# Optimization experiments

Measured on AMD Instinct MI355X. Metric: run time of the kernel, lower is better.

The kernel has to match this reference:

```python
import jax, jax.numpy as jnp
import numpy as np

WORLD_SIZE = 4
NUM_TOKENS = 1024
TOPK = 2
NUM_EXPERTS = 8
INTER_PER_RANK = 1024  # intermediate_size (4096) // world_size (4)
HIDDEN = 2048


def setup_inputs() -> dict:
    key = jax.random.key(0)
    k1, k2, k3 = jax.random.split(key, 3)
    # per-rank shard of expert intermediate activations, expanded (token, topk) order
    intermediate_states = jax.random.normal(
        k1, (WORLD_SIZE, NUM_TOKENS * TOPK, INTER_PER_RANK), dtype=jnp.float16)
    # per-rank shard of expert down-proj weights [rank, expert, inter_per_rank, hidden]
    w = (jax.random.normal(
        k2, (WORLD_SIZE, NUM_EXPERTS, INTER_PER_RANK, HIDDEN), dtype=jnp.float32) * 0.05
        ).astype(jnp.float16)
    router_logits = jax.random.normal(k3, (NUM_TOKENS, NUM_EXPERTS), dtype=jnp.float32)
    return {"intermediate_states": intermediate_states, "w": w,
            "router_logits": router_logits, "topk": TOPK}


def reference(intermediate_states, w, router_logits, topk):
    # intermediate_states: [R, T*topk, I_pr], w: [R, E, I_pr, H], router_logits: [T, E]
    R, TK, I = intermediate_states.shape
    _, E, _, H = w.shape
    T = TK // topk

    # top-k routing: softmax over the selected top-k logits (Mixtral-style gates)
    vals, idx = jax.lax.top_k(router_logits, topk)            # [T, topk]
    gate = jax.nn.softmax(vals, axis=-1)                      # [T, topk] fp32
    # combine weights per expanded token per expert: [T*topk, E]
    comb = (jax.nn.one_hot(idx, E, dtype=jnp.float32) * gate[..., None]).reshape(TK, E)

    # grouped GEMM (dense all-expert form) with fp32 accumulation; the einsum
    # simultaneously sums the per-rank partials (the "reduce" of reduce-scatter)
    x32 = intermediate_states.astype(jnp.float32)
    w32 = w.astype(jnp.float32)
    h_all = jnp.einsum('rti,reih->teh', x32, w32)             # [T*topk, E, H]
    y = jnp.einsum('teh,te->th', h_all, comb)                 # [T*topk, H]
    y = y.reshape(T, topk, H).sum(axis=1)                     # combine top-k -> [T, H]

    # "scatter" half of reduce-scatter: each rank keeps T//R contiguous tokens
    out = y.reshape(R, T // R, H).astype(intermediate_states.dtype)
    return out
```

## Files before the change

### kernel.cpp

```cpp
#include <hip/hip_runtime.h>
#include <hip/hip_bf16.h>

#define NTOK 1024
#define TKN  2048
#define NE   8
#define NRANK 4
#define IPR  1024
#define HD   2048
#define KD   4096
#define BM   256
#define BN   64
#define BK   64
#define KSPLIT 2
#define KPS  (KD / KSPLIT)
#define NIT  (KPS / BK)
#define XS   72
#define MAXTILES 16
#define NBL  (HD / BN)
#define NWG  (MAXTILES * NBL * KSPLIT)

typedef __bf16 bf16x8 __attribute__((ext_vector_type(8)));
typedef float f32x4 __attribute__((ext_vector_type(4)));
typedef unsigned short u16x8 __attribute__((ext_vector_type(8)));

static __device__ inline unsigned short f2b(float f) {
  return __builtin_bit_cast(unsigned short, __float2bfloat16(f));
}

__global__ __launch_bounds__(256) void zero_kernel(float* __restrict__ p) {
  size_t i = ((size_t)blockIdx.x * 256 + threadIdx.x) * 4;
  *reinterpret_cast<float4*>(p + i) = float4{0.f, 0.f, 0.f, 0.f};
}

__global__ void routing_kernel(const float* __restrict__ logits,
                               float* __restrict__ gate,
                               int* __restrict__ perm,
                               int* __restrict__ tile_e,
                               int* __restrict__ tile_r0,
                               int* __restrict__ tile_nr) {
  __shared__ int cnt[NE];
  __shared__ int cur[NE];
  const int tid = threadIdx.x;
  if (tid < NE) cnt[tid] = 0;
  __syncthreads();

  float l[NE];
#pragma unroll
  for (int e = 0; e < NE; ++e) l[e] = logits[tid * NE + e];

  float v0 = l[0]; int i0 = 0;
  float v1 = -3.4e38f; int i1 = 0;
#pragma unroll
  for (int e = 1; e < NE; ++e) {
    if (l[e] > v0) { v1 = v0; i1 = i0; v0 = l[e]; i0 = e; }
    else if (l[e] > v1) { v1 = l[e]; i1 = e; }
  }
  float e1  = expf(v1 - v0);
  float inv = 1.0f / (1.0f + e1);
  gate[2 * tid]     = inv;
  gate[2 * tid + 1] = e1 * inv;

  atomicAdd(&cnt[i0], 1);
  atomicAdd(&cnt[i1], 1);
  __syncthreads();

  if (tid == 0) {
    int run = 0, nt = 0;
    for (int e = 0; e < NE; ++e) {
      cur[e] = run;
      int c = cnt[e];
      for (int r0 = 0; r0 < c; r0 += BM) {
        tile_e[nt]  = e;
        tile_r0[nt] = run + r0;
        tile_nr[nt] = (c - r0 < BM) ? (c - r0) : BM;
        ++nt;
      }
      run += c;
    }
    for (; nt < MAXTILES; ++nt) tile_e[nt] = -1;
  }
  __syncthreads();

  int p0 = atomicAdd(&cur[i0], 1); perm[p0] = 2 * tid;
  int p1 = atomicAdd(&cur[i1], 1); perm[p1] = 2 * tid + 1;
}

__global__ __launch_bounds__(512, 4) void gemm_kernel(
    const float* __restrict__ x,
    const float* __restrict__ w,
    const int* __restrict__ perm,
    const int* __restrict__ tile_e,
    const int* __restrict__ tile_r0,
    const int* __restrict__ tile_nr,
    const float* __restrict__ gate,
    float* __restrict__ out) {
  const int id = blockIdx.x;
  const int sw = (id & 7) * (NWG / 8) + (id >> 3);
  const int tile = sw % MAXTILES;
  const int rem  = sw / MAXTILES;
  const int nb   = rem % NBL;
  const int ksp  = rem / NBL;

  const int e = tile_e[tile];
  if (e < 0) return;
  const int row0 = tile_r0[tile];
  const int nr   = tile_nr[tile];
  const int n0   = nb * BN;
  const int kbase = ksp * KPS;

  __shared__ unsigned short Xs[BM][XS];
  __shared__ unsigned short Ws[BN][XS];

  const int tid  = threadIdx.x;
  const int lane = tid & 63;
  const int wid  = tid >> 6;
  const int wr   = wid >> 1;
  const int wc   = wid & 1;

  const int xr = tid >> 3;
  const int xc = (tid & 7) << 3;
  int xtk[4];
#pragma unroll
  for (int p = 0; p < 4; ++p) {
    const int row = p * 64 + xr;
    xtk[p] = (row < nr) ? perm[row0 + row] : -1;
  }

  const int wn  = tid & 63;
  const int wkq = (tid >> 6) << 3;

  float4 xf[4][2];
  float  wv[8];

#define LOADREGS(KT) do {                                                        \
    const int r_  = (KT) >> 10;                                                  \
    const int i0_ = (KT) & 1023;                                                 \
    _Pragma("unroll")                                                            \
    for (int p_ = 0; p_ < 4; ++p_) {                                             \
      if (xtk[p_] >= 0) {                                                        \
        const float* sp_ = x + ((size_t)r_ * TKN + xtk[p_]) * IPR + i0_ + xc;    \
        xf[p_][0] = *reinterpret_cast<const float4*>(sp_);                       \
        xf[p_][1] = *reinterpret_cast<const float4*>(sp_ + 4);                   \
      } else {                                                                   \
        xf[p_][0] = float4{0.f, 0.f, 0.f, 0.f};                                  \
        xf[p_][1] = float4{0.f, 0.f, 0.f, 0.f};                                  \
      }                                                                          \
    }                                                                            \
    const float* wp_ = w + (((size_t)r_ * NE + e) * IPR + i0_ + wkq) * HD + n0 + wn; \
    _Pragma("unroll")                                                            \
    for (int j_ = 0; j_ < 8; ++j_) wv[j_] = wp_[(size_t)j_ * HD];                \
  } while (0)

  f32x4 acc[4][2];
#pragma unroll
  for (int a = 0; a < 4; ++a)
#pragma unroll
    for (int b = 0; b < 2; ++b) acc[a][b] = f32x4{0.f, 0.f, 0.f, 0.f};

  const int lrow = lane & 15;
  const int lk   = (lane >> 4) << 3;

  LOADREGS(kbase);

  for (int t = 0; t < NIT; ++t) {
    __syncthreads();

#pragma unroll
    for (int p = 0; p < 4; ++p) {
      u16x8 v;
      v[0] = f2b(xf[p][0].x); v[1] = f2b(xf[p][0].y);
      v[2] = f2b(xf[p][0].z); v[3] = f2b(xf[p][0].w);
      v[4] = f2b(xf[p][1].x); v[5] = f2b(xf[p][1].y);
      v[6] = f2b(xf[p][1].z); v[7] = f2b(xf[p][1].w);
      *reinterpret_cast<u16x8*>(&Xs[p * 64 + xr][xc]) = v;
    }
    {
      u16x8 a;
      a[0] = f2b(wv[0]); a[1] = f2b(wv[1]); a[2] = f2b(wv[2]); a[3] = f2b(wv[3]);
      a[4] = f2b(wv[4]); a[5] = f2b(wv[5]); a[6] = f2b(wv[6]); a[7] = f2b(wv[7]);
      *reinterpret_cast<u16x8*>(&Ws[wn][wkq]) = a;
    }
    __syncthreads();

    if (t + 1 < NIT) LOADREGS(kbase + (t + 1) * BK);

#pragma unroll
    for (int ks = 0; ks < 2; ++ks) {
      bf16x8 af[4], bfr[2];
#pragma unroll
      for (int mi = 0; mi < 4; ++mi)
        af[mi] = __builtin_bit_cast(bf16x8,
            *reinterpret_cast<const u16x8*>(&Xs[wr * 64 + mi * 16 + lrow][ks * 32 + lk]));
#pragma unroll
      for (int ni = 0; ni < 2; ++ni)
        bfr[ni] = __builtin_bit_cast(bf16x8,
            *reinterpret_cast<const u16x8*>(&Ws[wc * 32 + ni * 16 + lrow][ks * 32 + lk]));
#pragma unroll
      for (int mi = 0; mi < 4; ++mi)
#pragma unroll
        for (int ni = 0; ni < 2; ++ni)
          acc[mi][ni] = __builtin_amdgcn_mfma_f32_16x16x32_bf16(af[mi], bfr[ni], acc[mi][ni], 0, 0, 0);
    }
  }

  const int mb = (lane >> 4) << 2;
#pragma unroll
  for (int mi = 0; mi < 4; ++mi) {
#pragma unroll
    for (int q = 0; q < 4; ++q) {
      const int m = wr * 64 + mi * 16 + mb + q;
      if (m < nr) {
        const int tk = perm[row0 + m];
        const float g = gate[tk];
        float* dst = out + (size_t)(tk >> 1) * HD + n0 + wc * 32 + (lane & 15);
#pragma unroll
        for (int ni = 0; ni < 2; ++ni)
          atomicAdd(&dst[ni * 16], g * acc[mi][ni][q]);
      }
    }
  }
#undef LOADREGS
}

extern "C" void kernel_launch(void* const* d_in, const int* in_sizes, int n_in,
                              void* d_out, int out_size, void* d_ws, size_t ws_size,
                              hipStream_t stream) {
  const float* x      = (const float*)d_in[0];
  const float* w      = (const float*)d_in[1];
  const float* logits = (const float*)d_in[2];

  char* ws = (char*)d_ws;
  float* gate    = (float*)(ws + 0);
  int*   perm    = (int*)(ws + 8192);
  int*   tile_e  = (int*)(ws + 16384);
  int*   tile_r0 = (int*)(ws + 16384 + 256);
  int*   tile_nr = (int*)(ws + 16384 + 512);

  float* outf = (float*)d_out;

  zero_kernel<<<(NTOK * HD / 4) / 256, 256, 0, stream>>>(outf);
  routing_kernel<<<1, 1024, 0, stream>>>(logits, gate, perm, tile_e, tile_r0, tile_nr);
  gemm_kernel<<<NWG, 512, 0, stream>>>(x, w, perm, tile_e, tile_r0, tile_nr, gate, outf);
}
```

Baseline: 184.5 us.

## Widen N tile, convert to bf16 at load, replace atomics with workspace combine

Doubles the N tile width to 128 so each workgroup reuses its gathered X tile across more columns, halving the number of workgroups and the redundant X reads. The fp32-to-bf16 conversion moves into the global-load step so fewer registers are held across the compute phase. When enough workspace is available, each split-K/expert partial is stored plainly into a per-split expanded buffer, and a separate combine kernel applies the gates and sums. This replaces float atomics and the zero kernel, at the cost of writing and re-reading about 32 MB of workspace and launching one more kernel.

```diff
diff --git a/kernel.cpp b/kernel.cpp
--- a/kernel.cpp
+++ b/kernel.cpp
@@ -9,7 +9,7 @@
 #define HD   2048
 #define KD   4096
 #define BM   256
-#define BN   64
+#define BN   128
 #define BK   64
 #define KSPLIT 2
 #define KPS  (KD / KSPLIT)
@@ -18,6 +18,9 @@
 #define MAXTILES 16
 #define NBL  (HD / BN)
 #define NWG  (MAXTILES * NBL * KSPLIT)
+
+#define WS_YEXP_OFF 32768
+#define WS_NEED ((size_t)WS_YEXP_OFF + (size_t)KSPLIT * TKN * HD * 4)
 
 typedef __bf16 bf16x8 __attribute__((ext_vector_type(8)));
 typedef float f32x4 __attribute__((ext_vector_type(4)));
@@ -85,6 +88,7 @@
   int p1 = atomicAdd(&cur[i1], 1); perm[p1] = 2 * tid + 1;
 }
 
+template <int WSP>
 __global__ __launch_bounds__(512, 4) void gemm_kernel(
     const float* __restrict__ x,
     const float* __restrict__ w,
@@ -93,13 +97,13 @@
     const int* __restrict__ tile_r0,
     const int* __restrict__ tile_nr,
     const float* __restrict__ gate,
+    float* __restrict__ yexp,
     float* __restrict__ out) {
   const int id = blockIdx.x;
   const int sw = (id & 7) * (NWG / 8) + (id >> 3);
-  const int tile = sw % MAXTILES;
-  const int rem  = sw / MAXTILES;
-  const int nb   = rem % NBL;
-  const int ksp  = rem / NBL;
+  const int tile = sw & (MAXTILES - 1);
+  const int nb   = (sw >> 4) & (NBL - 1);
+  const int ksp  = sw >> 8;
 
   const int e = tile_e[tile];
   if (e < 0) return;
@@ -126,11 +130,11 @@
     xtk[p] = (row < nr) ? perm[row0 + row] : -1;
   }
 
-  const int wn  = tid & 63;
-  const int wkq = (tid >> 6) << 3;
-
-  float4 xf[4][2];
-  float  wv[8];
+  const int wn  = tid & 127;
+  const int wkg = (tid >> 7) << 4;
+
+  u16x8 xpk[4];
+  u16x8 wpk[2];
 
 #define LOADREGS(KT) do {                                                        \
     const int r_  = (KT) >> 10;                                                  \
@@ -139,23 +143,40 @@
     for (int p_ = 0; p_ < 4; ++p_) {                                             \
       if (xtk[p_] >= 0) {                                                        \
         const float* sp_ = x + ((size_t)r_ * TKN + xtk[p_]) * IPR + i0_ + xc;    \
-        xf[p_][0] = *reinterpret_cast<const float4*>(sp_);                       \
-        xf[p_][1] = *reinterpret_cast<const float4*>(sp_ + 4);                   \
+        float4 f0_ = *reinterpret_cast<const float4*>(sp_);                      \
+        float4 f1_ = *reinterpret_cast<const float4*>(sp_ + 4);                  \
+        u16x8 v_;                                                                \
+        v_[0] = f2b(f0_.x); v_[1] = f2b(f0_.y); v_[2] = f2b(f0_.z);              \
+        v_[3] = f2b(f0_.w); v_[4] = f2b(f1_.x); v_[5] = f2b(f1_.y);              \
+        v_[6] = f2b(f1_.z); v_[7] = f2b(f1_.w);                                  \
+        xpk[p_] = v_;                                                            \
       } else {                                                                   \
-        xf[p_][0] = float4{0.f, 0.f, 0.f, 0.f};                                  \
-        xf[p_][1] = float4{0.f, 0.f, 0.f, 0.f};                                  \
+        xpk[p_] = u16x8{0, 0, 0, 0, 0, 0, 0, 0};                                 \
       }                                                                          \
     }                                                                            \
-    const float* wp_ = w + (((size_t)r_ * NE + e) * IPR + i0_ + wkq) * HD + n0 + wn; \
+    const float* wp_ = w + (((size_t)r_ * NE + e) * IPR + i0_ + wkg) * HD + n0 + wn; \
     _Pragma("unroll")                                                            \
-    for (int j_ = 0; j_ < 8; ++j_) wv[j_] = wp_[(size_t)j_ * HD];                \
+    for (int h_ = 0; h_ < 2; ++h_) {                                             \
+      float t0_ = wp_[(size_t)(h_ * 8 + 0) * HD];                                \
+      float t1_ = wp_[(size_t)(h_ * 8 + 1) * HD];                                \
+      float t2_ = wp_[(size_t)(h_ * 8 + 2) * HD];                                \
+      float t3_ = wp_[(size_t)(h_ * 8 + 3) * HD];                                \
+      float t4_ = wp_[(size_t)(h_ * 8 + 4) * HD];                                \
+      float t5_ = wp_[(size_t)(h_ * 8 + 5) * HD];                                \
+      float t6_ = wp_[(size_t)(h_ * 8 + 6) * HD];                                \
+      float t7_ = wp_[(size_t)(h_ * 8 + 7) * HD];                                \
+      u16x8 v_;                                                                  \
+      v_[0] = f2b(t0_); v_[1] = f2b(t1_); v_[2] = f2b(t2_); v_[3] = f2b(t3_);    \
+      v_[4] = f2b(t4_); v_[5] = f2b(t5_); v_[6] = f2b(t6_); v_[7] = f2b(t7_);    \
+      wpk[h_] = v_;                                                              \
+    }                                                                            \
   } while (0)
 
-  f32x4 acc[4][2];
+  f32x4 acc[4][4];
 #pragma unroll
   for (int a = 0; a < 4; ++a)
 #pragma unroll
-    for (int b = 0; b < 2; ++b) acc[a][b] = f32x4{0.f, 0.f, 0.f, 0.f};
+    for (int b = 0; b < 4; ++b) acc[a][b] = f32x4{0.f, 0.f, 0.f, 0.f};
 
   const int lrow = lane & 15;
   const int lk   = (lane >> 4) << 3;
@@ -166,39 +187,29 @@
     __syncthreads();
 
 #pragma unroll
-    for (int p = 0; p < 4; ++p) {
-      u16x8 v;
-      v[0] = f2b(xf[p][0].x); v[1] = f2b(xf[p][0].y);
-      v[2] = f2b(xf[p][0].z); v[3] = f2b(xf[p][0].w);
-      v[4] = f2b(xf[p][1].x); v[5] = f2b(xf[p][1].y);
-      v[6] = f2b(xf[p][1].z); v[7] = f2b(xf[p][1].w);
-      *reinterpret_cast<u16x8*>(&Xs[p * 64 + xr][xc]) = v;
-    }
-    {
-      u16x8 a;
-      a[0] = f2b(wv[0]); a[1] = f2b(wv[1]); a[2] = f2b(wv[2]); a[3] = f2b(wv[3]);
-      a[4] = f2b(wv[4]); a[5] = f2b(wv[5]); a[6] = f2b(wv[6]); a[7] = f2b(wv[7]);
-      *reinterpret_cast<u16x8*>(&Ws[wn][wkq]) = a;
-    }
+    for (int p = 0; p < 4; ++p)
+      *reinterpret_cast<u16x8*>(&Xs[p * 64 + xr][xc]) = xpk[p];
+    *reinterpret_cast<u16x8*>(&Ws[wn][wkg])     = wpk[0];
+    *reinterpret_cast<u16x8*>(&Ws[wn][wkg + 8]) = wpk[1];
     __syncthreads();
 
     if (t + 1 < NIT) LOADREGS(kbase + (t + 1) * BK);
 
 #pragma unroll
     for (int ks = 0; ks < 2; ++ks) {
-      bf16x8 af[4], bfr[2];
+      bf16x8 af[4], bfr[4];
 #pragma unroll
       for (int mi = 0; mi < 4; ++mi)
         af[mi] = __builtin_bit_cast(bf16x8,
             *reinterpret_cast<const u16x8*>(&Xs[wr * 64 + mi * 16 + lrow][ks * 32 + lk]));
 #pragma unroll
-      for (int ni = 0; ni < 2; ++ni)
+      for (int ni = 0; ni < 4; ++ni)
         bfr[ni] = __builtin_bit_cast(bf16x8,
-            *reinterpret_cast<const u16x8*>(&Ws[wc * 32 + ni * 16 + lrow][ks * 32 + lk]));
+            *reinterpret_cast<const u16x8*>(&Ws[wc * 64 + ni * 16 + lrow][ks * 32 + lk]));
 #pragma unroll
       for (int mi = 0; mi < 4; ++mi)
 #pragma unroll
-        for (int ni = 0; ni < 2; ++ni)
+        for (int ni = 0; ni < 4; ++ni)
           acc[mi][ni] = __builtin_amdgcn_mfma_f32_16x16x32_bf16(af[mi], bfr[ni], acc[mi][ni], 0, 0, 0);
     }
   }
@@ -211,15 +222,48 @@
       const int m = wr * 64 + mi * 16 + mb + q;
       if (m < nr) {
         const int tk = perm[row0 + m];
-        const float g = gate[tk];
-        float* dst = out + (size_t)(tk >> 1) * HD + n0 + wc * 32 + (lane & 15);
-#pragma unroll
-        for (int ni = 0; ni < 2; ++ni)
-          atomicAdd(&dst[ni * 16], g * acc[mi][ni][q]);
+        if (WSP) {
+          float* dst = yexp + ((size_t)ksp * TKN + tk) * HD + n0 + wc * 64 + lrow;
+#pragma unroll
+          for (int ni = 0; ni < 4; ++ni)
+            dst[ni * 16] = acc[mi][ni][q];
+        } else {
+          const float g = gate[tk];
+          float* dst = out + (size_t)(tk >> 1) * HD + n0 + wc * 64 + lrow;
+#pragma unroll
+          for (int ni = 0; ni < 4; ++ni)
+            atomicAdd(&dst[ni * 16], g * acc[mi][ni][q]);
+        }
       }
     }
   }
 #undef LOADREGS
+}
+
+__global__ __launch_bounds__(256) void combine_kernel(const float* __restrict__ yexp,
+                                                      const float* __restrict__ gate,
+                                                      float* __restrict__ out) {
+  const int idx = blockIdx.x * 256 + threadIdx.x;
+  const int t  = idx >> 9;
+  const int h4 = (idx & 511) << 2;
+  const float g0 = gate[2 * t];
+  const float g1 = gate[2 * t + 1];
+
+  const float* y00 = yexp + ((size_t)(2 * t)) * HD + h4;
+  const float* y01 = yexp + ((size_t)(2 * t + 1)) * HD + h4;
+  const float* y10 = yexp + ((size_t)TKN + 2 * t) * HD + h4;
+  const float* y11 = yexp + ((size_t)TKN + 2 * t + 1) * HD + h4;
+  float4 a0 = *reinterpret_cast<const float4*>(y00);
+  float4 a1 = *reinterpret_cast<const float4*>(y01);
+  float4 b0 = *reinterpret_cast<const float4*>(y10);
+  float4 b1 = *reinterpret_cast<const float4*>(y11);
+
+  float4 o;
+  o.x = g0 * (a0.x + b0.x) + g1 * (a1.x + b1.x);
+  o.y = g0 * (a0.y + b0.y) + g1 * (a1.y + b1.y);
+  o.z = g0 * (a0.z + b0.z) + g1 * (a1.z + b1.z);
+  o.w = g0 * (a0.w + b0.w) + g1 * (a1.w + b1.w);
+  *reinterpret_cast<float4*>(out + (size_t)t * HD + h4) = o;
 }
 
 extern "C" void kernel_launch(void* const* d_in, const int* in_sizes, int n_in,
@@ -235,10 +279,19 @@
   int*   tile_e  = (int*)(ws + 16384);
   int*   tile_r0 = (int*)(ws + 16384 + 256);
   int*   tile_nr = (int*)(ws + 16384 + 512);
+  float* yexp    = (float*)(ws + WS_YEXP_OFF);
 
   float* outf = (float*)d_out;
 
-  zero_kernel<<<(NTOK * HD / 4) / 256, 256, 0, stream>>>(outf);
   routing_kernel<<<1, 1024, 0, stream>>>(logits, gate, perm, tile_e, tile_r0, tile_nr);
-  gemm_kernel<<<NWG, 512, 0, stream>>>(x, w, perm, tile_e, tile_r0, tile_nr, gate, outf);
-}
+
+  if (ws_size >= WS_NEED) {
+    gemm_kernel<1><<<NWG, 512, 0, stream>>>(x, w, perm, tile_e, tile_r0, tile_nr,
+                                            gate, yexp, outf);
+    combine_kernel<<<(NTOK * HD / 4) / 256, 256, 0, stream>>>(yexp, gate, outf);
+  } else {
+    zero_kernel<<<(NTOK * HD / 4) / 256, 256, 0, stream>>>(outf);
+    gemm_kernel<0><<<NWG, 512, 0, stream>>>(x, w, perm, tile_e, tile_r0, tile_nr,
+                                            gate, yexp, outf);
+  }
+}
```

Measured after the change: 216.2 us. +17.1%, slower.
